# Performance work log

Measured on AMD Instinct MI355X. Metric: run time of the kernel, lower is better.

The kernel has to match this reference:

```python
import jax, jax.numpy as jnp
import numpy as np
from jax import lax

HEADS = 4
DIM = 64
GATE_HID = 16


def setup_inputs() -> dict:
    key = jax.random.key(0)
    ks = jax.random.split(key, 12)
    b, c, h, w = 2, DIM, 48, 48
    s = 0.05
    x = jax.random.normal(ks[0], (b, c, h, w), jnp.float32)
    Wqkv = jax.random.normal(ks[1], (3 * c, c), jnp.float32) * s
    bqkv = jax.random.normal(ks[2], (3 * c,), jnp.float32) * s
    Wpos = jax.random.normal(ks[3], (3 * c, 1, 3, 3), jnp.float32) * s
    bpos = jax.random.normal(ks[4], (3 * c,), jnp.float32) * s
    Wg1 = jax.random.normal(ks[5], (GATE_HID, 1), jnp.float32) * 0.5
    bg1 = jax.random.normal(ks[6], (GATE_HID,), jnp.float32) * 0.1
    Wg2 = jax.random.normal(ks[7], (1, GATE_HID), jnp.float32) * 0.5
    bg2 = jax.random.normal(ks[8], (1,), jnp.float32) * 0.1
    Wproj = jax.random.normal(ks[9], (c, c), jnp.float32) * s
    bproj = jax.random.normal(ks[10], (c,), jnp.float32) * s
    return {"x": x, "Wqkv": Wqkv, "bqkv": bqkv, "Wpos": Wpos, "bpos": bpos,
            "Wg1": Wg1, "bg1": bg1, "Wg2": Wg2, "bg2": bg2,
            "Wproj": Wproj, "bproj": bproj}


def _forward(x, Wqkv, bqkv, Wpos, bpos, Wg1, bg1, Wg2, bg2, Wproj, bproj):
    b, c, h, w = x.shape
    n = h * w
    heads = HEADS
    hd = c // heads
    scale = hd ** -0.5
    # qkv 1x1 conv then 3x3 depthwise positional conv
    qkv = jnp.einsum('bchw,oc->bohw', x, Wqkv) + bqkv[None, :, None, None]
    qkv = lax.conv_general_dilated(
        qkv, Wpos, window_strides=(1, 1), padding='SAME',
        feature_group_count=3 * c,
        dimension_numbers=('NCHW', 'OIHW', 'NCHW')) + bpos[None, :, None, None]
    q, k, v = jnp.split(qkv, 3, axis=1)

    def to_heads(t):
        # [b,c,h,w] -> [b,heads,n,hd]
        return t.reshape(b, c, n).transpose(0, 2, 1).reshape(b, n, heads, hd).transpose(0, 2, 1, 3)

    q, k, v = to_heads(q), to_heads(k), to_heads(v)
    attn = jnp.einsum('bhid,bhjd->bhij', q, k) * scale  # [b,heads,n,n]
    prob = jax.nn.softmax(attn, axis=-1)
    entropy = -(prob * jnp.log(jnp.clip(prob, 1e-12))).sum(-1).mean(-1)  # [b,heads]
    # entropy gate: sigmoid(fc2(relu(fc1(e)))) * 0.9 + 0.1
    hgate = jax.nn.relu(entropy[..., None] @ Wg1.T + bg1)  # [b,heads,16]
    ratio = jax.nn.sigmoid(hgate @ Wg2.T + bg2)[..., 0] * 0.9 + 0.1  # [b,heads]
    # dynamic per-(batch,head) top-k along rows via rank threshold
    keep = jnp.clip(jnp.ceil(ratio * n).astype(jnp.int32), 1, n)  # [b,heads]
    sorted_desc = -jnp.sort(-attn, axis=-1)  # [b,heads,n,n]
    idx = jnp.broadcast_to((keep - 1)[:, :, None, None], (b, heads, n, 1))
    thresh = jnp.take_along_axis(sorted_desc, idx, axis=-1)  # [b,heads,n,1]
    sparse = jnp.where(attn >= thresh, attn, -jnp.inf)
    p = jax.nn.softmax(sparse, axis=-1)
    out = jnp.einsum('bhij,bhjd->bhid', p, v)  # [b,heads,n,hd]
    out = out.transpose(0, 2, 1, 3).reshape(b, n, c)
    out = out @ Wproj.T + bproj
    return out.transpose(0, 2, 1).reshape(b, c, h, w)


def reference(x, Wqkv, bqkv, Wpos, bpos, Wg1, bg1, Wg2, bg2, Wproj, bproj):
    return _forward(x, Wqkv, bqkv, Wpos, bpos, Wg1, bg1, Wg2, bg2, Wproj, bproj)
```

## Files before the change

### kernel.cpp

```cpp
#include <hip/hip_runtime.h>
#include <hip/hip_fp16.h>


typedef _Float16 half8_t __attribute__((ext_vector_type(8)));
typedef float floatx4 __attribute__((ext_vector_type(4)));

union HU { unsigned short s; _Float16 h; };
__device__ __forceinline__ _Float16 ubits_h(unsigned short u) {
  HU c; c.s = u; return c.h;
}
__device__ __forceinline__ _Float16 key_h(unsigned k) {
  unsigned short u = (k & 0x8000u) ? (unsigned short)(k & 0x7FFFu)
                                   : (unsigned short)((~k) & 0xFFFFu);
  return ubits_h(u);
}

__device__ __forceinline__ uint2 hist_select(const unsigned* hist, int lane,
                                             unsigned keepN) {
  uint4 cc = ((const uint4*)hist)[lane];
  unsigned inc = cc.x + cc.y + cc.z + cc.w;
#pragma unroll
  for (int off = 1; off < 64; off <<= 1) {
    unsigned t = __shfl_up(inc, off);
    if (lane >= off) inc += t;
  }
  unsigned total = __shfl(inc, 63);
  unsigned above = total - inc;
  unsigned a3 = above;
  unsigned a2 = a3 + cc.w;
  unsigned a1 = a2 + cc.z;
  unsigned a0 = a1 + cc.y;
  bool has = false;
  unsigned B_l = 0, A_l = 0;
  if (a3 < keepN && a3 + cc.w >= keepN) { has = true; B_l = lane * 4 + 3; A_l = a3; }
  else if (a2 < keepN && a2 + cc.z >= keepN) { has = true; B_l = lane * 4 + 2; A_l = a2; }
  else if (a1 < keepN && a1 + cc.y >= keepN) { has = true; B_l = lane * 4 + 1; A_l = a1; }
  else if (a0 < keepN && a0 + cc.x >= keepN) { has = true; B_l = lane * 4 + 0; A_l = a0; }
  unsigned long long m = __ballot(has);
  int src = __ffsll(m) - 1;
  unsigned B = __shfl(B_l, src);
  unsigned run = __shfl(A_l, src);
  return make_uint2(B, run);
}

__global__ __launch_bounds__(256) void k_qkv(const float* __restrict__ x,
                                             const float* __restrict__ W,
                                             const float* __restrict__ bias,
                                             float* __restrict__ out,
                                             float* __restrict__ ent) {
  if (blockIdx.x == 0 && threadIdx.x < 8) ent[threadIdx.x] = 0.f;
  int blk = blockIdx.x;
  int chunk = blk % 9;
  int og = (blk / 9) % 48;
  int b = blk / (9 * 48);
  int o0 = og * 4;
  int pos = chunk * 256 + threadIdx.x;
  const float* xb = x + b * 64 * 2304 + pos;
  const float* w0 = W + (o0 + 0) * 64;
  const float* w1 = W + (o0 + 1) * 64;
  const float* w2 = W + (o0 + 2) * 64;
  const float* w3 = W + (o0 + 3) * 64;
  float a0 = bias[o0 + 0], a1 = bias[o0 + 1];
  float a2 = bias[o0 + 2], a3 = bias[o0 + 3];
#pragma unroll
  for (int c = 0; c < 64; c++) {
    float xv = xb[c * 2304];
    a0 = fmaf(w0[c], xv, a0);
    a1 = fmaf(w1[c], xv, a1);
    a2 = fmaf(w2[c], xv, a2);
    a3 = fmaf(w3[c], xv, a3);
  }
  out[(b * 192 + o0 + 0) * 2304 + pos] = a0;
  out[(b * 192 + o0 + 1) * 2304 + pos] = a1;
  out[(b * 192 + o0 + 2) * 2304 + pos] = a2;
  out[(b * 192 + o0 + 3) * 2304 + pos] = a3;
}

__global__ __launch_bounds__(256) void k_dw(const float* __restrict__ qkv,
                                            const float* __restrict__ Wpos,
                                            const float* __restrict__ bpos,
                                            _Float16* __restrict__ q2,
                                            _Float16* __restrict__ k2,
                                            _Float16* __restrict__ vt) {
  __shared__ float smem[8][384];
  int blk = blockIdx.x;
  int chunk = blk % 9;
  int half = (blk / 9) % 2;
  int sel = (blk / 18) % 3;
  int head = (blk / 54) % 4;
  int b = blk / 216;
  int chbase = sel * 64 + head * 16 + half * 8;
  int bh = b * 4 + head;
  int tid = threadIdx.x;
  int p0 = chunk * 256;
  int baserow = p0 / 48;
  int rA = min(max(baserow - 1, 0), 40);

  const float* src = qkv + (size_t)(b * 192 + chbase) * 2304;
#pragma unroll
  for (int l = 0; l < 12; l++) {
    int idx = tid + l * 256;
    int ch = idx / 384;
    int off = idx - ch * 384;
    int rr = off / 48;
    int cc = off - rr * 48;
    smem[ch][off] = src[(size_t)ch * 2304 + (rA + rr) * 48 + cc];
  }
  __syncthreads();

  int pos = p0 + tid;
  int yy = pos / 48, xx = pos - yy * 48;
  int ry = yy - rA;
  float accv[8];
#pragma unroll
  for (int d = 0; d < 8; d++) {
    const float* w = Wpos + (chbase + d) * 9;
    float a = bpos[chbase + d];
#pragma unroll
    for (int dy = -1; dy <= 1; dy++) {
      int y2 = yy + dy;
      if ((unsigned)y2 < 48u) {
#pragma unroll
        for (int dx = -1; dx <= 1; dx++) {
          int x2 = xx + dx;
          if ((unsigned)x2 < 48u)
            a = fmaf(w[(dy + 1) * 3 + (dx + 1)], smem[d][(ry + dy) * 48 + x2],
                     a);
        }
      }
    }
    accv[d] = a;
  }

  if (sel == 2) {
#pragma unroll
    for (int d = 0; d < 8; d++)
      vt[((size_t)bh * 16 + half * 8 + d) * 2304 + pos] = (_Float16)accv[d];
  } else {
    _Float16 h1[8], h2[8];
#pragma unroll
    for (int d = 0; d < 8; d++) {
      float a = (sel == 0) ? accv[d] * 0.25f : accv[d];
      h1[d] = (_Float16)a;
      h2[d] = (_Float16)(a - (float)h1[d]);
    }
    _Float16* dst = ((sel == 0) ? q2 : k2) + ((size_t)bh * 2304 + pos) * 32;
    *(uint4*)(dst + half * 8) = *(uint4*)&h1[0];
    *(uint4*)(dst + 16 + half * 8) = *(uint4*)&h2[0];
  }
}

template <bool STORE>
__global__ __launch_bounds__(256) void k_ent_t(const _Float16* __restrict__ q2,
                                               const _Float16* __restrict__ k2,
                                               float* __restrict__ ent,
                                               _Float16* __restrict__ lgH) {
  __shared__ __align__(16) _Float16 tBuf[4][16][72];
  __shared__ float sWv[4][16], uWv[4][16];

  int blk = blockIdx.x;
  int rowtile = blk % 144;
  int bh = blk / 144;
  int row0 = rowtile * 16;
  int tid = threadIdx.x, lane = tid & 63, wave = tid >> 6;
  int m16 = lane & 15, quad = lane >> 4;

  const half8_t* q2v =
      (const half8_t*)(q2 + ((size_t)bh * 2304 + row0 + m16) * 32);
  half8_t A1 = q2v[quad];
  half8_t zh = {};
  half8_t A2 = (lane < 32) ? A1 : zh;
  const half8_t* kbase = (const half8_t*)(k2 + (size_t)bh * 2304 * 32);

  float s[4] = {0.f, 0.f, 0.f, 0.f}, u[4] = {0.f, 0.f, 0.f, 0.f};
  for (int g = 0; g < 9; g++) {
#pragma unroll
    for (int tt = 0; tt < 4; tt++) {
      int t = g * 4 + tt;
      int col = wave * 576 + t * 16 + m16;
      const half8_t* kk = kbase + (size_t)col * 4;
      half8_t b1 = kk[quad & 1];
      half8_t b2 = kk[2 + (quad & 1)];
      floatx4 acc = {};
      acc = __builtin_amdgcn_mfma_f32_16x16x32_f16(A2, b2, acc, 0, 0, 0);
      acc = __builtin_amdgcn_mfma_f32_16x16x32_f16(A1, b1, acc, 0, 0, 0);
#pragma unroll
      for (int i = 0; i < 4; i++) {
        if (STORE) tBuf[wave][quad * 4 + i][tt * 16 + m16] = (_Float16)acc[i];
        float e = __expf(acc[i]);
        s[i] += e;
        u[i] = fmaf(acc[i], e, u[i]);
      }
    }
    if (STORE) {
      __syncthreads();
      int rb = lane >> 3, seg = lane & 7;
#pragma unroll
      for (int it = 0; it < 2; it++) {
        int rr = it * 8 + rb;
        uint4 vv = *(const uint4*)&tBuf[wave][rr][seg * 8];
        *(uint4*)(lgH + ((size_t)bh * 2304 + row0 + rr) * 2304 + wave * 576 +
                  g * 64 + seg * 8) = vv;
      }
      __syncthreads();
    }
  }
#pragma unroll
  for (int off = 1; off < 16; off <<= 1) {
#pragma unroll
    for (int i = 0; i < 4; i++) {
      s[i] += __shfl_xor(s[i], off);
      u[i] += __shfl_xor(u[i], off);
    }
  }
  if (m16 == 0) {
#pragma unroll
    for (int i = 0; i < 4; i++) {
      sWv[wave][quad * 4 + i] = s[i];
      uWv[wave][quad * 4 + i] = u[i];
    }
  }
  __syncthreads();
  if (tid < 16) {
    float S = sWv[0][tid] + sWv[1][tid] + sWv[2][tid] + sWv[3][tid];
    float U = uWv[0][tid] + uWv[1][tid] + uWv[2][tid] + uWv[3][tid];
    float er = __logf(S) - U / S;
    er += __shfl_xor(er, 1);
    er += __shfl_xor(er, 2);
    er += __shfl_xor(er, 4);
    er += __shfl_xor(er, 8);
    if (tid == 0) atomicAdd(&ent[bh], er);
  }
}

#define EXPPACKW(W0, IT)                                              \
  {                                                                   \
    _Float16 h0 = ubits_h((unsigned short)(wb[W0 + 0] & 0xFFFFu));    \
    _Float16 h1 = ubits_h((unsigned short)(wb[W0 + 0] >> 16));        \
    _Float16 h2 = ubits_h((unsigned short)(wb[W0 + 1] & 0xFFFFu));    \
    _Float16 h3 = ubits_h((unsigned short)(wb[W0 + 1] >> 16));        \
    _Float16 h4 = ubits_h((unsigned short)(wb[W0 + 2] & 0xFFFFu));    \
    _Float16 h5 = ubits_h((unsigned short)(wb[W0 + 2] >> 16));        \
    _Float16 h6 = ubits_h((unsigned short)(wb[W0 + 3] & 0xFFFFu));    \
    _Float16 h7 = ubits_h((unsigned short)(wb[W0 + 3] >> 16));        \
    float p0 = (h0 >= th_h) ? __expf((float)h0) : 0.f;                \
    float p1 = (h1 >= th_h) ? __expf((float)h1) : 0.f;                \
    float p2 = (h2 >= th_h) ? __expf((float)h2) : 0.f;                \
    float p3 = (h3 >= th_h) ? __expf((float)h3) : 0.f;                \
    float p4 = (h4 >= th_h) ? __expf((float)h4) : 0.f;                \
    float p5 = (h5 >= th_h) ? __expf((float)h5) : 0.f;                \
    float p6 = (h6 >= th_h) ? __expf((float)h6) : 0.f;                \
    float p7 = (h7 >= th_h) ? __expf((float)h7) : 0.f;                \
    sp += ((p0 + p1) + (p2 + p3)) + ((p4 + p5) + (p6 + p7));          \
    uint4 o;                                                          \
    __half2 q0 = __floats2half2_rn(p0, p1); o.x = *(unsigned*)&q0;    \
    __half2 q1 = __floats2half2_rn(p2, p3); o.y = *(unsigned*)&q1;    \
    __half2 q2h = __floats2half2_rn(p4, p5); o.z = *(unsigned*)&q2h;  \
    __half2 q3 = __floats2half2_rn(p6, p7); o.w = *(unsigned*)&q3;    \
    prow4[lane + IT * 64] = o;                                        \
  }

template <bool CACHED>
__global__ __launch_bounds__(256, 6) void k_attn_t(
    const _Float16* __restrict__ q2, const _Float16* __restrict__ k2,
    const _Float16* __restrict__ vt, const _Float16* __restrict__ lgH,
    const float* __restrict__ ent, const float* __restrict__ Wg1,
    const float* __restrict__ bg1, const float* __restrict__ Wg2,
    const float* __restrict__ bg2, float* __restrict__ oh) {
  __shared__ __align__(16) _Float16 pbuf[4][2320];
  __shared__ float sS[4];
  __shared__ __align__(16) float redSh[4][64];

  int a = blockIdx.x;
  int v8 = a & 7;
  int idx = a >> 3;
  int q = idx & 3;
  int pi = idx >> 2;
  int bh = pi / 18;
  int rowtile = v8 + (pi % 18) * 8;
  int rowblk = rowtile * 4 + q;
  int row0 = rowblk * 4;
  int tid = threadIdx.x, lane = tid & 63, wave = tid >> 6;

  float eAvg = ent[bh] * (1.f / 2304.f);
  float gacc = bg2[0];
#pragma unroll
  for (int i = 0; i < 16; i++) {
    float h = fmaxf(fmaf(eAvg, Wg1[i], bg1[i]), 0.f);
    gacc = fmaf(h, Wg2[i], gacc);
  }
  float ratio = 0.9f / (1.f + __expf(-gacc)) + 0.1f;
  int kp = (int)ceilf(ratio * 2304.f);
  unsigned keep = (unsigned)min(max(kp, 1), 2304);

  unsigned wb[18];
  if (CACHED) {
    const _Float16* src = lgH + ((size_t)bh * 2304 + row0 + wave) * 2304;
    const uint4* s4 = (const uint4*)src;
    uint4 r0 = s4[lane];
    uint4 r1 = s4[lane + 64];
    uint4 r2 = s4[lane + 128];
    uint4 r3 = s4[lane + 192];
    uint2 r4 = *(const uint2*)(src + 2048 + lane * 4);
    wb[0] = r0.x; wb[1] = r0.y; wb[2] = r0.z; wb[3] = r0.w;
    wb[4] = r1.x; wb[5] = r1.y; wb[6] = r1.z; wb[7] = r1.w;
    wb[8] = r2.x; wb[9] = r2.y; wb[10] = r2.z; wb[11] = r2.w;
    wb[12] = r3.x; wb[13] = r3.y; wb[14] = r3.z; wb[15] = r3.w;
    wb[16] = r4.x; wb[17] = r4.y;
  } else {
    int m16 = lane & 15, quad = lane >> 4;
    const half8_t* q2v =
        (const half8_t*)(q2 + ((size_t)bh * 2304 + row0 + (m16 & 3)) * 32);
    half8_t A1 = q2v[quad];
    half8_t zh = {};
    half8_t A2 = (lane < 32) ? A1 : zh;
    const half8_t* kbase = (const half8_t*)(k2 + (size_t)bh * 2304 * 32);
#pragma unroll 4
    for (int t = 0; t < 36; t++) {
      int ct = wave * 36 + t;
      int col = ct * 16 + m16;
      const half8_t* kk = kbase + (size_t)col * 4;
      half8_t b1 = kk[quad & 1];
      half8_t b2 = kk[2 + (quad & 1)];
      floatx4 acc = {};
      acc = __builtin_amdgcn_mfma_f32_16x16x32_f16(A2, b2, acc, 0, 0, 0);
      acc = __builtin_amdgcn_mfma_f32_16x16x32_f16(A1, b1, acc, 0, 0, 0);
      if (lane < 16) {
#pragma unroll
        for (int i = 0; i < 4; i++) pbuf[i][ct * 16 + lane] = (_Float16)acc[i];
      }
    }
    __syncthreads();
    const _Float16* src = pbuf[wave];
    const uint4* s4 = (const uint4*)src;
    uint4 r0 = s4[lane];
    uint4 r1 = s4[lane + 64];
    uint4 r2 = s4[lane + 128];
    uint4 r3 = s4[lane + 192];
    uint2 r4 = *(const uint2*)(src + 2048 + lane * 4);
    wb[0] = r0.x; wb[1] = r0.y; wb[2] = r0.z; wb[3] = r0.w;
    wb[4] = r1.x; wb[5] = r1.y; wb[6] = r1.z; wb[7] = r1.w;
    wb[8] = r2.x; wb[9] = r2.y; wb[10] = r2.z; wb[11] = r2.w;
    wb[12] = r3.x; wb[13] = r3.y; wb[14] = r3.z; wb[15] = r3.w;
    wb[16] = r4.x; wb[17] = r4.y;
  }

  _Float16 th_h;
  {
    unsigned* hist = (unsigned*)&pbuf[wave][0];
    unsigned kb[18];
#pragma unroll
    for (int i = 0; i < 18; i++)
      kb[i] = wb[i] ^ (((wb[i] >> 15) & 0x00010001u) * 0x7FFFu + 0x80008000u);

#pragma unroll
    for (int i = 0; i < 4; i++) hist[lane + i * 64] = 0u;
#pragma unroll
    for (int i = 0; i < 18; i++) {
      atomicAdd(&hist[(kb[i] >> 8) & 0xFFu], 1u);
      atomicAdd(&hist[kb[i] >> 24], 1u);
    }
    uint2 s1 = hist_select(hist, lane, keep);
    unsigned B = s1.x;
    unsigned keep2 = keep - s1.y;

#pragma unroll
    for (int i = 0; i < 4; i++) hist[lane + i * 64] = 0u;
#pragma unroll
    for (int i = 0; i < 18; i++) {
      unsigned klo = kb[i] & 0xFFFFu;
      unsigned khi = kb[i] >> 16;
      if ((klo >> 8) == B) atomicAdd(&hist[klo & 0xFFu], 1u);
      if ((khi >> 8) == B) atomicAdd(&hist[khi & 0xFFu], 1u);
    }
    uint2 s2 = hist_select(hist, lane, keep2);
    unsigned K = (B << 8) | s2.x;
    th_h = key_h(K);
  }

  {
    float sp = 0.f;
    uint4* prow4 = (uint4*)pbuf[wave];
    EXPPACKW(0, 0);
    EXPPACKW(4, 1);
    EXPPACKW(8, 2);
    EXPPACKW(12, 3);
    {
      _Float16 h0 = ubits_h((unsigned short)(wb[16] & 0xFFFFu));
      _Float16 h1 = ubits_h((unsigned short)(wb[16] >> 16));
      _Float16 h2 = ubits_h((unsigned short)(wb[17] & 0xFFFFu));
      _Float16 h3 = ubits_h((unsigned short)(wb[17] >> 16));
      float p0 = (h0 >= th_h) ? __expf((float)h0) : 0.f;
      float p1 = (h1 >= th_h) ? __expf((float)h1) : 0.f;
      float p2 = (h2 >= th_h) ? __expf((float)h2) : 0.f;
      float p3 = (h3 >= th_h) ? __expf((float)h3) : 0.f;
      sp += (p0 + p1) + (p2 + p3);
      uint2 o;
      __half2 q0 = __floats2half2_rn(p0, p1); o.x = *(unsigned*)&q0;
      __half2 q1 = __floats2half2_rn(p2, p3); o.y = *(unsigned*)&q1;
      *(uint2*)(pbuf[wave] + 2048 + lane * 4) = o;
    }
#pragma unroll
    for (int off = 1; off < 64; off <<= 1) sp += __shfl_xor(sp, off);
    if (lane == 0) sS[wave] = sp;
  }
  __syncthreads();

  {
    int m16 = lane & 15, quad = lane >> 4;
    const _Float16* vrow = vt + ((size_t)bh * 16 + m16) * 2304;
    const _Float16* prow = pbuf[m16 & 3];
    int jb0 = wave * 576 + quad * 8;
    floatx4 acc = {};
#pragma unroll 6
    for (int t = 0; t < 18; t++) {
      int jb = jb0 + t * 32;
      half8_t a2 = *(const half8_t*)&prow[jb];
      half8_t b2 = *(const half8_t*)&vrow[jb];
      acc = __builtin_amdgcn_mfma_f32_16x16x32_f16(a2, b2, acc, 0, 0, 0);
    }
    if (lane < 16) {
      *(floatx4*)&redSh[wave][m16 * 4] = acc;
    }
  }
  __syncthreads();
  if (tid < 64) {
    int r = tid & 3, d = tid >> 2;
    float s2 = redSh[0][d * 4 + r] + redSh[1][d * 4 + r] +
               redSh[2][d * 4 + r] + redSh[3][d * 4 + r];
    oh[((size_t)(bh * 2304 + row0 + r)) * 16 + d] = s2 / sS[r];
  }
}

__global__ __launch_bounds__(256) void k_proj(const float* __restrict__ oh,
                                              const float* __restrict__ Wp,
                                              const float* __restrict__ bp,
                                              float* __restrict__ out) {
  int blk = blockIdx.x;
  int chunk = blk % 9;
  int cog = (blk / 9) % 16;
  int b = blk / (9 * 16);
  int co0 = cog * 4;
  int pos = chunk * 256 + threadIdx.x;
  float a0 = bp[co0 + 0], a1 = bp[co0 + 1], a2 = bp[co0 + 2], a3 = bp[co0 + 3];
#pragma unroll
  for (int head = 0; head < 4; head++) {
    const float4* op =
        (const float4*)(oh + ((size_t)((b * 4 + head) * 2304 + pos)) * 16);
#pragma unroll
    for (int p = 0; p < 4; p++) {
      float4 o4 = op[p];
#pragma unroll
      for (int i = 0; i < 4; i++) {
        const float* wr = Wp + (co0 + i) * 64 + head * 16 + p * 4;
        float* ai = (i == 0) ? &a0 : ((i == 1) ? &a1 : ((i == 2) ? &a2 : &a3));
        *ai = fmaf(wr[0], o4.x, *ai);
        *ai = fmaf(wr[1], o4.y, *ai);
        *ai = fmaf(wr[2], o4.z, *ai);
        *ai = fmaf(wr[3], o4.w, *ai);
      }
    }
  }
  out[(b * 64 + co0 + 0) * 2304 + pos] = a0;
  out[(b * 64 + co0 + 1) * 2304 + pos] = a1;
  out[(b * 64 + co0 + 2) * 2304 + pos] = a2;
  out[(b * 64 + co0 + 3) * 2304 + pos] = a3;
}

extern "C" void kernel_launch(void* const* d_in, const int* in_sizes, int n_in,
                              void* d_out, int out_size, void* d_ws,
                              size_t ws_size, hipStream_t stream) {
  const float* x    = (const float*)d_in[0];
  const float* Wqkv = (const float*)d_in[1];
  const float* bqkv = (const float*)d_in[2];
  const float* Wpos = (const float*)d_in[3];
  const float* bpos = (const float*)d_in[4];
  const float* Wg1  = (const float*)d_in[5];
  const float* bg1  = (const float*)d_in[6];
  const float* Wg2  = (const float*)d_in[7];
  const float* bg2  = (const float*)d_in[8];
  const float* Wpr  = (const float*)d_in[9];
  const float* bpr  = (const float*)d_in[10];
  float* out = (float*)d_out;

  const size_t lgBytes = (size_t)8 * 2304 * 2304 * 2;
  const size_t baseBytes = (size_t)(884736 + 294912 + 8) * 4 +
                           (size_t)(2 * 589824 + 294912) * 2;
  bool cached = ws_size >= lgBytes + baseBytes;

  char* base = (char*)d_ws;
  _Float16* lgH = nullptr;
  if (cached) {
    lgH = (_Float16*)base;
    base += lgBytes;
  }
  float* qkv_raw = (float*)base;
  float* oh = qkv_raw + 884736;
  float* ent = oh + 294912;
  _Float16* q2 = (_Float16*)(ent + 8);
  _Float16* k2 = q2 + 589824;
  _Float16* vt = k2 + 589824;

  hipLaunchKernelGGL(k_qkv, dim3(2 * 48 * 9), dim3(256), 0, stream,
                     x, Wqkv, bqkv, qkv_raw, ent);
  hipLaunchKernelGGL(k_dw, dim3(432), dim3(256), 0, stream,
                     qkv_raw, Wpos, bpos, q2, k2, vt);
  if (cached) {
    hipLaunchKernelGGL((k_ent_t<true>), dim3(8 * 144), dim3(256), 0, stream,
                       q2, k2, ent, lgH);
    hipLaunchKernelGGL((k_attn_t<true>), dim3(8 * 576), dim3(256), 0, stream,
                       q2, k2, vt, lgH, ent, Wg1, bg1, Wg2, bg2, oh);
  } else {
    hipLaunchKernelGGL((k_ent_t<false>), dim3(8 * 144), dim3(256), 0, stream,
                       q2, k2, ent, lgH);
    hipLaunchKernelGGL((k_attn_t<false>), dim3(8 * 576), dim3(256), 0, stream,
                       q2, k2, vt, lgH, ent, Wg1, bg1, Wg2, bg2, oh);
  }
  hipLaunchKernelGGL(k_proj, dim3(2 * 16 * 9), dim3(256), 0, stream,
                     oh, Wpr, bpr, out);
}
```

Before: 194.0 us.

## Recompute logits per 16-row tile in LDS instead of caching them globally

The cached path, which wrote every fp16 QK logit to a large global workspace in the entropy kernel and read it back in the attention kernel, is removed. The attention kernel now uses 512 threads per block over 16 query rows. It recomputes those rows' logits with MFMA into a swizzled LDS tile, then runs top-k threshold selection with packed 16-bit histogram counters, and does the PV product from the same LDS tile. This avoids the round trip of roughly 85 MB through global memory, at the cost of recomputing QK and of large LDS use that limits occupancy. The exp/sum loop also evaluates several exponentials twice.

```diff
diff --git a/kernel.cpp b/kernel.cpp
--- a/kernel.cpp
+++ b/kernel.cpp
@@ -15,10 +15,12 @@
   return ubits_h(u);
 }
 
-__device__ __forceinline__ uint2 hist_select(const unsigned* hist, int lane,
-                                             unsigned keepN) {
-  uint4 cc = ((const uint4*)hist)[lane];
-  unsigned inc = cc.x + cc.y + cc.z + cc.w;
+__device__ __forceinline__ uint2 hist_select_p(const unsigned* h, int lane,
+                                               unsigned keepN) {
+  uint2 w = ((const uint2*)h)[lane];
+  unsigned c0 = w.x & 0xFFFFu, c1 = w.x >> 16;
+  unsigned c2 = w.y & 0xFFFFu, c3 = w.y >> 16;
+  unsigned inc = c0 + c1 + c2 + c3;
 #pragma unroll
   for (int off = 1; off < 64; off <<= 1) {
     unsigned t = __shfl_up(inc, off);
@@ -27,20 +29,18 @@
   unsigned total = __shfl(inc, 63);
   unsigned above = total - inc;
   unsigned a3 = above;
-  unsigned a2 = a3 + cc.w;
-  unsigned a1 = a2 + cc.z;
-  unsigned a0 = a1 + cc.y;
+  unsigned a2 = a3 + c3;
+  unsigned a1 = a2 + c2;
+  unsigned a0 = a1 + c1;
   bool has = false;
   unsigned B_l = 0, A_l = 0;
-  if (a3 < keepN && a3 + cc.w >= keepN) { has = true; B_l = lane * 4 + 3; A_l = a3; }
-  else if (a2 < keepN && a2 + cc.z >= keepN) { has = true; B_l = lane * 4 + 2; A_l = a2; }
-  else if (a1 < keepN && a1 + cc.y >= keepN) { has = true; B_l = lane * 4 + 1; A_l = a1; }
-  else if (a0 < keepN && a0 + cc.x >= keepN) { has = true; B_l = lane * 4 + 0; A_l = a0; }
+  if (a3 < keepN && a3 + c3 >= keepN) { has = true; B_l = lane * 4 + 3; A_l = a3; }
+  else if (a2 < keepN && a2 + c2 >= keepN) { has = true; B_l = lane * 4 + 2; A_l = a2; }
+  else if (a1 < keepN && a1 + c1 >= keepN) { has = true; B_l = lane * 4 + 1; A_l = a1; }
+  else if (a0 < keepN && a0 + c0 >= keepN) { has = true; B_l = lane * 4 + 0; A_l = a0; }
   unsigned long long m = __ballot(has);
   int src = __ffsll(m) - 1;
-  unsigned B = __shfl(B_l, src);
-  unsigned run = __shfl(A_l, src);
-  return make_uint2(B, run);
+  return make_uint2(__shfl(B_l, src), __shfl(A_l, src));
 }
 
 __global__ __launch_bounds__(256) void k_qkv(const float* __restrict__ x,
@@ -233,54 +233,23 @@
   }
 }
 
-#define EXPPACKW(W0, IT)                                              \
-  {                                                                   \
-    _Float16 h0 = ubits_h((unsigned short)(wb[W0 + 0] & 0xFFFFu));    \
-    _Float16 h1 = ubits_h((unsigned short)(wb[W0 + 0] >> 16));        \
-    _Float16 h2 = ubits_h((unsigned short)(wb[W0 + 1] & 0xFFFFu));    \
-    _Float16 h3 = ubits_h((unsigned short)(wb[W0 + 1] >> 16));        \
-    _Float16 h4 = ubits_h((unsigned short)(wb[W0 + 2] & 0xFFFFu));    \
-    _Float16 h5 = ubits_h((unsigned short)(wb[W0 + 2] >> 16));        \
-    _Float16 h6 = ubits_h((unsigned short)(wb[W0 + 3] & 0xFFFFu));    \
-    _Float16 h7 = ubits_h((unsigned short)(wb[W0 + 3] >> 16));        \
-    float p0 = (h0 >= th_h) ? __expf((float)h0) : 0.f;                \
-    float p1 = (h1 >= th_h) ? __expf((float)h1) : 0.f;                \
-    float p2 = (h2 >= th_h) ? __expf((float)h2) : 0.f;                \
-    float p3 = (h3 >= th_h) ? __expf((float)h3) : 0.f;                \
-    float p4 = (h4 >= th_h) ? __expf((float)h4) : 0.f;                \
-    float p5 = (h5 >= th_h) ? __expf((float)h5) : 0.f;                \
-    float p6 = (h6 >= th_h) ? __expf((float)h6) : 0.f;                \
-    float p7 = (h7 >= th_h) ? __expf((float)h7) : 0.f;                \
-    sp += ((p0 + p1) + (p2 + p3)) + ((p4 + p5) + (p6 + p7));          \
-    uint4 o;                                                          \
-    __half2 q0 = __floats2half2_rn(p0, p1); o.x = *(unsigned*)&q0;    \
-    __half2 q1 = __floats2half2_rn(p2, p3); o.y = *(unsigned*)&q1;    \
-    __half2 q2h = __floats2half2_rn(p4, p5); o.z = *(unsigned*)&q2h;  \
-    __half2 q3 = __floats2half2_rn(p6, p7); o.w = *(unsigned*)&q3;    \
-    prow4[lane + IT * 64] = o;                                        \
-  }
-
-template <bool CACHED>
-__global__ __launch_bounds__(256, 6) void k_attn_t(
+__global__ __launch_bounds__(512, 2) void k_attn_f(
     const _Float16* __restrict__ q2, const _Float16* __restrict__ k2,
-    const _Float16* __restrict__ vt, const _Float16* __restrict__ lgH,
-    const float* __restrict__ ent, const float* __restrict__ Wg1,
-    const float* __restrict__ bg1, const float* __restrict__ Wg2,
-    const float* __restrict__ bg2, float* __restrict__ oh) {
-  __shared__ __align__(16) _Float16 pbuf[4][2320];
-  __shared__ float sS[4];
-  __shared__ __align__(16) float redSh[4][64];
-
-  int a = blockIdx.x;
-  int v8 = a & 7;
-  int idx = a >> 3;
-  int q = idx & 3;
-  int pi = idx >> 2;
-  int bh = pi / 18;
-  int rowtile = v8 + (pi % 18) * 8;
-  int rowblk = rowtile * 4 + q;
-  int row0 = rowblk * 4;
+    const _Float16* __restrict__ vt, const float* __restrict__ ent,
+    const float* __restrict__ Wg1, const float* __restrict__ bg1,
+    const float* __restrict__ Wg2, const float* __restrict__ bg2,
+    float* __restrict__ oh) {
+  __shared__ __align__(16) _Float16 lg[16 * 2304];
+  __shared__ unsigned hist[8][128];
+  __shared__ float sS[16];
+
+  int blk = blockIdx.x;
+  int bh = blk & 7;
+  int tile = blk >> 3;
+  int row0 = tile * 16;
   int tid = threadIdx.x, lane = tid & 63, wave = tid >> 6;
+  int m16 = lane & 15, quad = lane >> 4;
+  char* lgc = (char*)lg;
 
   float eAvg = ent[bh] * (1.f / 2304.f);
   float gacc = bg2[0];
@@ -293,98 +262,118 @@
   int kp = (int)ceilf(ratio * 2304.f);
   unsigned keep = (unsigned)min(max(kp, 1), 2304);
 
-  unsigned wb[18];
-  if (CACHED) {
-    const _Float16* src = lgH + ((size_t)bh * 2304 + row0 + wave) * 2304;
-    const uint4* s4 = (const uint4*)src;
-    uint4 r0 = s4[lane];
-    uint4 r1 = s4[lane + 64];
-    uint4 r2 = s4[lane + 128];
-    uint4 r3 = s4[lane + 192];
-    uint2 r4 = *(const uint2*)(src + 2048 + lane * 4);
-    wb[0] = r0.x; wb[1] = r0.y; wb[2] = r0.z; wb[3] = r0.w;
-    wb[4] = r1.x; wb[5] = r1.y; wb[6] = r1.z; wb[7] = r1.w;
-    wb[8] = r2.x; wb[9] = r2.y; wb[10] = r2.z; wb[11] = r2.w;
-    wb[12] = r3.x; wb[13] = r3.y; wb[14] = r3.z; wb[15] = r3.w;
-    wb[16] = r4.x; wb[17] = r4.y;
-  } else {
-    int m16 = lane & 15, quad = lane >> 4;
+  {
     const half8_t* q2v =
-        (const half8_t*)(q2 + ((size_t)bh * 2304 + row0 + (m16 & 3)) * 32);
+        (const half8_t*)(q2 + ((size_t)bh * 2304 + row0 + m16) * 32);
     half8_t A1 = q2v[quad];
     half8_t zh = {};
     half8_t A2 = (lane < 32) ? A1 : zh;
     const half8_t* kbase = (const half8_t*)(k2 + (size_t)bh * 2304 * 32);
-#pragma unroll 4
-    for (int t = 0; t < 36; t++) {
-      int ct = wave * 36 + t;
-      int col = ct * 16 + m16;
+#pragma unroll 2
+    for (int t = 0; t < 18; t++) {
+      int col = wave * 288 + t * 16 + m16;
       const half8_t* kk = kbase + (size_t)col * 4;
       half8_t b1 = kk[quad & 1];
       half8_t b2 = kk[2 + (quad & 1)];
       floatx4 acc = {};
       acc = __builtin_amdgcn_mfma_f32_16x16x32_f16(A2, b2, acc, 0, 0, 0);
       acc = __builtin_amdgcn_mfma_f32_16x16x32_f16(A1, b1, acc, 0, 0, 0);
-      if (lane < 16) {
-#pragma unroll
-        for (int i = 0; i < 4; i++) pbuf[i][ct * 16 + lane] = (_Float16)acc[i];
-      }
-    }
-    __syncthreads();
-    const _Float16* src = pbuf[wave];
-    const uint4* s4 = (const uint4*)src;
-    uint4 r0 = s4[lane];
-    uint4 r1 = s4[lane + 64];
-    uint4 r2 = s4[lane + 128];
-    uint4 r3 = s4[lane + 192];
-    uint2 r4 = *(const uint2*)(src + 2048 + lane * 4);
-    wb[0] = r0.x; wb[1] = r0.y; wb[2] = r0.z; wb[3] = r0.w;
-    wb[4] = r1.x; wb[5] = r1.y; wb[6] = r1.z; wb[7] = r1.w;
-    wb[8] = r2.x; wb[9] = r2.y; wb[10] = r2.z; wb[11] = r2.w;
-    wb[12] = r3.x; wb[13] = r3.y; wb[14] = r3.z; wb[15] = r3.w;
-    wb[16] = r4.x; wb[17] = r4.y;
-  }
-
-  _Float16 th_h;
-  {
-    unsigned* hist = (unsigned*)&pbuf[wave][0];
+#pragma unroll
+      for (int i = 0; i < 4; i++) {
+        int row = quad * 4 + i;
+        *(_Float16*)(lgc + row * 4608 +
+                     ((col * 2) ^ (((row >> 2) & 3) << 5))) =
+            (_Float16)acc[i];
+      }
+    }
+  }
+  __syncthreads();
+
+#pragma unroll 1
+  for (int rr = 0; rr < 2; rr++) {
+    int r = wave * 2 + rr;
+    char* rb = lgc + r * 4608;
+    int sw = ((r >> 2) & 3) << 5;
+    uint4 q0 = *(const uint4*)(rb + ((lane * 16) ^ sw));
+    uint4 q1 = *(const uint4*)(rb + ((1024 + lane * 16) ^ sw));
+    uint4 q2r = *(const uint4*)(rb + ((2048 + lane * 16) ^ sw));
+    uint4 q3 = *(const uint4*)(rb + ((3072 + lane * 16) ^ sw));
+    uint2 q4 = *(const uint2*)(rb + ((4096 + lane * 8) ^ sw));
+    unsigned wb[18] = {q0.x, q0.y, q0.z, q0.w, q1.x, q1.y, q1.z, q1.w,
+                       q2r.x, q2r.y, q2r.z, q2r.w, q3.x, q3.y, q3.z, q3.w,
+                       q4.x, q4.y};
     unsigned kb[18];
 #pragma unroll
     for (int i = 0; i < 18; i++)
       kb[i] = wb[i] ^ (((wb[i] >> 15) & 0x00010001u) * 0x7FFFu + 0x80008000u);
 
-#pragma unroll
-    for (int i = 0; i < 4; i++) hist[lane + i * 64] = 0u;
+    unsigned* h = hist[wave];
+    h[lane] = 0u;
+    h[lane + 64] = 0u;
 #pragma unroll
     for (int i = 0; i < 18; i++) {
-      atomicAdd(&hist[(kb[i] >> 8) & 0xFFu], 1u);
-      atomicAdd(&hist[kb[i] >> 24], 1u);
-    }
-    uint2 s1 = hist_select(hist, lane, keep);
+      unsigned b1 = (kb[i] >> 8) & 0xFFu;
+      unsigned b2 = kb[i] >> 24;
+      atomicAdd(&h[b1 >> 1], 1u << ((b1 & 1) << 4));
+      atomicAdd(&h[b2 >> 1], 1u << ((b2 & 1) << 4));
+    }
+    uint2 s1 = hist_select_p(h, lane, keep);
     unsigned B = s1.x;
     unsigned keep2 = keep - s1.y;
 
-#pragma unroll
-    for (int i = 0; i < 4; i++) hist[lane + i * 64] = 0u;
+    h[lane] = 0u;
+    h[lane + 64] = 0u;
 #pragma unroll
     for (int i = 0; i < 18; i++) {
       unsigned klo = kb[i] & 0xFFFFu;
       unsigned khi = kb[i] >> 16;
-      if ((klo >> 8) == B) atomicAdd(&hist[klo & 0xFFu], 1u);
-      if ((khi >> 8) == B) atomicAdd(&hist[khi & 0xFFu], 1u);
-    }
-    uint2 s2 = hist_select(hist, lane, keep2);
-    unsigned K = (B << 8) | s2.x;
-    th_h = key_h(K);
-  }
-
-  {
+      if ((klo >> 8) == B) {
+        unsigned lb = klo & 0xFFu;
+        atomicAdd(&h[lb >> 1], 1u << ((lb & 1) << 4));
+      }
+      if ((khi >> 8) == B) {
+        unsigned lb = khi & 0xFFu;
+        atomicAdd(&h[lb >> 1], 1u << ((lb & 1) << 4));
+      }
+    }
+    uint2 s2 = hist_select_p(h, lane, keep2);
+    _Float16 th_h = key_h((B << 8) | s2.x);
+
     float sp = 0.f;
-    uint4* prow4 = (uint4*)pbuf[wave];
-    EXPPACKW(0, 0);
-    EXPPACKW(4, 1);
-    EXPPACKW(8, 2);
-    EXPPACKW(12, 3);
+#pragma unroll
+    for (int g = 0; g < 4; g++) {
+      uint4 o;
+      unsigned ow[4];
+#pragma unroll
+      for (int wj = 0; wj < 4; wj++) {
+        unsigned w = wb[g * 4 + wj];
+        _Float16 hlo = ubits_h((unsigned short)(w & 0xFFFFu));
+        _Float16 hhi = ubits_h((unsigned short)(w >> 16));
+        float plo = (hlo >= th_h) ? __expf((float)hlo) : 0.f;
+        float phi = (hhi >= th_h) ? __expf((float)hhi) : 0.f;
+        __half2 hp = __floats2half2_rn(plo, phi);
+        ow[wj] = *(unsigned*)&hp;
+        if (wj == 0) sp += ((plo + phi));
+      }
+      o.x = ow[0]; o.y = ow[1]; o.z = ow[2]; o.w = ow[3];
+      *(uint4*)(rb + (((g * 1024) + lane * 16) ^ sw)) = o;
+      {
+        _Float16 h2a = ubits_h((unsigned short)(wb[g * 4 + 1] & 0xFFFFu));
+        _Float16 h2b = ubits_h((unsigned short)(wb[g * 4 + 1] >> 16));
+        _Float16 h3a = ubits_h((unsigned short)(wb[g * 4 + 2] & 0xFFFFu));
+        _Float16 h3b = ubits_h((unsigned short)(wb[g * 4 + 2] >> 16));
+        _Float16 h4a = ubits_h((unsigned short)(wb[g * 4 + 3] & 0xFFFFu));
+        _Float16 h4b = ubits_h((unsigned short)(wb[g * 4 + 3] >> 16));
+        float p2 = (h2a >= th_h) ? __expf((float)h2a) : 0.f;
+        float p3 = (h2b >= th_h) ? __expf((float)h2b) : 0.f;
+        float p4 = (h3a >= th_h) ? __expf((float)h3a) : 0.f;
+        float p5 = (h3b >= th_h) ? __expf((float)h3b) : 0.f;
+        float p6 = (h4a >= th_h) ? __expf((float)h4a) : 0.f;
+        float p7 = (h4b >= th_h) ? __expf((float)h4b) : 0.f;
+        sp += (p2 + p3);
+        sp += (p4 + p5) + (p6 + p7);
+      }
+    }
     {
       _Float16 h0 = ubits_h((unsigned short)(wb[16] & 0xFFFFu));
       _Float16 h1 = ubits_h((unsigned short)(wb[16] >> 16));
@@ -396,38 +385,43 @@
       float p3 = (h3 >= th_h) ? __expf((float)h3) : 0.f;
       sp += (p0 + p1) + (p2 + p3);
       uint2 o;
-      __half2 q0 = __floats2half2_rn(p0, p1); o.x = *(unsigned*)&q0;
-      __half2 q1 = __floats2half2_rn(p2, p3); o.y = *(unsigned*)&q1;
-      *(uint2*)(pbuf[wave] + 2048 + lane * 4) = o;
+      __half2 hp0 = __floats2half2_rn(p0, p1); o.x = *(unsigned*)&hp0;
+      __half2 hp1 = __floats2half2_rn(p2, p3); o.y = *(unsigned*)&hp1;
+      *(uint2*)(rb + ((4096 + lane * 8) ^ sw)) = o;
     }
 #pragma unroll
     for (int off = 1; off < 64; off <<= 1) sp += __shfl_xor(sp, off);
-    if (lane == 0) sS[wave] = sp;
-  }
-  __syncthreads();
-
-  {
-    int m16 = lane & 15, quad = lane >> 4;
+    if (lane == 0) sS[r] = sp;
+  }
+  __syncthreads();
+
+  floatx4 acc = {};
+  if (wave < 4) {
     const _Float16* vrow = vt + ((size_t)bh * 16 + m16) * 2304;
-    const _Float16* prow = pbuf[m16 & 3];
+    const char* pr = lgc + m16 * 4608;
+    int sw2 = ((m16 >> 2) & 3) << 5;
     int jb0 = wave * 576 + quad * 8;
-    floatx4 acc = {};
 #pragma unroll 6
     for (int t = 0; t < 18; t++) {
       int jb = jb0 + t * 32;
-      half8_t a2 = *(const half8_t*)&prow[jb];
+      half8_t a2 = *(const half8_t*)(pr + ((jb * 2) ^ sw2));
       half8_t b2 = *(const half8_t*)&vrow[jb];
       acc = __builtin_amdgcn_mfma_f32_16x16x32_f16(a2, b2, acc, 0, 0, 0);
     }
-    if (lane < 16) {
-      *(floatx4*)&redSh[wave][m16 * 4] = acc;
-    }
-  }
-  __syncthreads();
-  if (tid < 64) {
-    int r = tid & 3, d = tid >> 2;
-    float s2 = redSh[0][d * 4 + r] + redSh[1][d * 4 + r] +
-               redSh[2][d * 4 + r] + redSh[3][d * 4 + r];
+  }
+  __syncthreads();
+  float* red = (float*)lg;
+  if (wave < 4) {
+#pragma unroll
+    for (int i = 0; i < 4; i++)
+      red[wave * 256 + (quad * 4 + i) * 16 + m16] = acc[i];
+  }
+  __syncthreads();
+  if (tid < 256) {
+    int r = tid >> 4;
+    float s2 = red[0 * 256 + tid] + red[1 * 256 + tid] +
+               red[2 * 256 + tid] + red[3 * 256 + tid];
+    int d = tid & 15;
     oh[((size_t)(bh * 2304 + row0 + r)) * 16 + d] = s2 / sS[r];
   }
 }
@@ -483,17 +477,7 @@
   const float* bpr  = (const float*)d_in[10];
   float* out = (float*)d_out;
 
-  const size_t lgBytes = (size_t)8 * 2304 * 2304 * 2;
-  const size_t baseBytes = (size_t)(884736 + 294912 + 8) * 4 +
-                           (size_t)(2 * 589824 + 294912) * 2;
-  bool cached = ws_size >= lgBytes + baseBytes;
-
   char* base = (char*)d_ws;
-  _Float16* lgH = nullptr;
-  if (cached) {
-    lgH = (_Float16*)base;
-    base += lgBytes;
-  }
   float* qkv_raw = (float*)base;
   float* oh = qkv_raw + 884736;
   float* ent = oh + 294912;
@@ -505,17 +489,10 @@
                      x, Wqkv, bqkv, qkv_raw, ent);
   hipLaunchKernelGGL(k_dw, dim3(432), dim3(256), 0, stream,
                      qkv_raw, Wpos, bpos, q2, k2, vt);
-  if (cached) {
-    hipLaunchKernelGGL((k_ent_t<true>), dim3(8 * 144), dim3(256), 0, stream,
-                       q2, k2, ent, lgH);
-    hipLaunchKernelGGL((k_attn_t<true>), dim3(8 * 576), dim3(256), 0, stream,
-                       q2, k2, vt, lgH, ent, Wg1, bg1, Wg2, bg2, oh);
-  } else {
-    hipLaunchKernelGGL((k_ent_t<false>), dim3(8 * 144), dim3(256), 0, stream,
-                       q2, k2, ent, lgH);
-    hipLaunchKernelGGL((k_attn_t<false>), dim3(8 * 576), dim3(256), 0, stream,
-                       q2, k2, vt, lgH, ent, Wg1, bg1, Wg2, bg2, oh);
-  }
+  hipLaunchKernelGGL((k_ent_t<false>), dim3(8 * 144), dim3(256), 0, stream,
+                     q2, k2, ent, (_Float16*)nullptr);
+  hipLaunchKernelGGL(k_attn_f, dim3(1152), dim3(512), 0, stream,
+                     q2, k2, vt, ent, Wg1, bg1, Wg2, bg2, oh);
   hipLaunchKernelGGL(k_proj, dim3(2 * 16 * 9), dim3(256), 0, stream,
                      oh, Wpr, bpr, out);
 }
```

New measurement: 200.9 us. 1.04x slower.
